# Performance work log

Hardware: AMD Instinct MI355X
Metric: run time of the kernel (lower is better)

## Reference

```python
import jax, jax.numpy as jnp
import numpy as np

VOCAB = 32000
HID = 1024


def _gru_cell(Wih, Whh, bih, bhh, h, x):
    # PyTorch GRU gate order: r, z, n
    gx = Wih @ x + bih          # [3H]
    gh = Whh @ h + bhh          # [3H]
    H = h.shape[0]
    r = jax.nn.sigmoid(gx[:H] + gh[:H])
    z = jax.nn.sigmoid(gx[H:2 * H] + gh[H:2 * H])
    n = jnp.tanh(gx[2 * H:] + r * gh[2 * H:])
    return (1.0 - z) * n + z * h


def setup_inputs() -> dict:
    key = jax.random.key(0)
    ks = jax.random.split(key, 13)
    S = 512
    T = 512
    s = 1.0 / np.sqrt(HID)
    u = lambda k, shape: jax.random.uniform(k, shape, jnp.float32, -s, s)
    return {
        "inputs": jax.random.randint(ks[0], (S,), 0, VOCAB, jnp.int32),
        "targets": jax.random.randint(ks[1], (T,), 0, VOCAB, jnp.int32),
        "emb": jax.random.normal(ks[2], (VOCAB, HID), jnp.float32),
        "enc_Wih": u(ks[3], (3 * HID, HID)),
        "enc_Whh": u(ks[4], (3 * HID, HID)),
        "enc_bih": u(ks[5], (3 * HID,)),
        "enc_bhh": u(ks[6], (3 * HID,)),
        "dec_Wih": u(ks[7], (3 * HID, HID)),
        "dec_Whh": u(ks[8], (3 * HID, HID)),
        "dec_bih": u(ks[9], (3 * HID,)),
        "dec_bhh": u(ks[10], (3 * HID,)),
        "proj_W": u(ks[11], (VOCAB, HID)),
        "proj_b": u(ks[12], (VOCAB,)),
    }


def reference(inputs, targets, emb, enc_Wih, enc_Whh, enc_bih, enc_bhh,
              dec_Wih, dec_Whh, dec_bih, dec_bhh, proj_W, proj_b):
    # Encoder: scan GRU over embedded source tokens (batch=1, state [H])
    src_emb = emb[inputs]  # [S,H]
    h0 = jnp.zeros((HID,), src_emb.dtype)

    def enc_step(h, x):
        return _gru_cell(enc_Wih, enc_Whh, enc_bih, enc_bhh, h, x), None

    enc_state, _ = jax.lax.scan(enc_step, h0, src_emb)

    # Decoder: teacher forcing; input token at step i is 0 (start) then targets[i-1]
    dec_tokens = jnp.concatenate([jnp.zeros((1,), targets.dtype), targets[:-1]])
    dec_emb = emb[dec_tokens]  # [T,H]

    def dec_step(h, x):
        h_new = _gru_cell(dec_Wih, dec_Whh, dec_bih, dec_bhh, h, x)
        return h_new, h_new

    _, dec_hs = jax.lax.scan(dec_step, enc_state, dec_emb)  # [T,H]

    # Projection to vocab logits (single GEMM over all timesteps)
    logits = dec_hs @ proj_W.T + proj_b  # [T,V]
    return logits
```

## Files before the change

kernel.cpp:

```cpp
#include <hip/hip_runtime.h>
#include <cstdint>
#include <cstddef>

#define H 1024
#define SEQ 512
#define THREEH 3072
#define VOCABN 32000
#define NBLK 64
#define NWORK 192
#define HPB 16

#define HBIAS 2.0f
#define HVALID 0.5f

template <int CTRL>
__device__ __forceinline__ float dpp_add(float v) {
    return v + __int_as_float(__builtin_amdgcn_update_dpp(
        0, __float_as_int(v), CTRL, 0xF, 0xF, true));
}
__device__ __forceinline__ float row16_sum(float v) {
    v = dpp_add<0xB1>(v);
    v = dpp_add<0x4E>(v);
    v = dpp_add<0x124>(v);
    v = dpp_add<0x128>(v);
    return v;
}

__device__ void rnn_path(int blk, int tid, float* smem,
    const float* __restrict__ eWhh, const float* __restrict__ ebhh,
    const float* __restrict__ dWhh, const float* __restrict__ dbhh,
    const float* __restrict__ gxe, const float* __restrict__ gxd,
    float* __restrict__ enc_t, float* __restrict__ dec_t,
    const float* __restrict__ fe, const float* __restrict__ fd)
{
    const int wave = tid >> 6;
    const int lane = tid & 63;
    const int g = lane >> 4;
    const int p = lane & 15;
    const int i0 = blk * HPB;
    const int myidx = i0 + 4 * wave + g;

    float* hs0 = smem;
    float* hs1 = smem + H;

    float4 wreg[3][16];
    float br, bz, bn;
    float hown = 0.f;

    auto load_w = [&](const float* __restrict__ W, const float* __restrict__ b) {
        float ws[3];
#pragma unroll
        for (int gate = 0; gate < 3; ++gate) {
            const float* base = W + (size_t)(gate * H + myidx) * H + 64 * p;
            float s = 0.f;
#pragma unroll
            for (int k = 0; k < 16; ++k) {
                float4 w = *(const float4*)(base + 4 * ((k + p) & 15));
                wreg[gate][k] = w;
                s += w.x + w.y + w.z + w.w;
            }
            ws[gate] = s;
        }
        br = b[myidx]         - HBIAS * row16_sum(ws[0]);
        bz = b[H + myidx]     - HBIAS * row16_sum(ws[1]);
        bn = b[2 * H + myidx] - HBIAS * row16_sum(ws[2]);
    };

    load_w(eWhh, ebhh);

    for (int step = 0; step < 2 * SEQ; ++step) {
        const bool dec = step >= SEQ;
        const int t = dec ? step - SEQ : step;
        if (dec && t == 0) load_w(dWhh, dbhh);

        if ((t & 63) == 0) {
            const float* fl = (dec ? fd : fe) + (t >> 6) * 64
                              + (lane < 48 ? lane : 47);
            for (;;) {
                float f = __hip_atomic_load(fl,
                    __ATOMIC_RELAXED, __HIP_MEMORY_SCOPE_AGENT);
                if (__all(f > HVALID)) break;
                __builtin_amdgcn_s_sleep(4);
            }
            __builtin_amdgcn_fence(__ATOMIC_ACQUIRE, "agent");
        }

        const float* gx = dec ? gxd : gxe;
        float* tb_out = (dec ? dec_t : enc_t) + (size_t)t * H;
        float* hb = (step & 1) ? hs1 : hs0;

        const float* gxp = gx + (size_t)t * THREEH + myidx;
        float gxr = gxp[0];
        float gxz = gxp[H];
        float gxn = gxp[2 * H];

        if (step == 0) {
            *(float4*)&hb[wave * 256 + lane * 4] =
                float4{HBIAS, HBIAS, HBIAS, HBIAS};
        } else {
            const float* tb_prev =
                (step <= SEQ) ? enc_t + (size_t)(step - 1) * H
                              : dec_t + (size_t)(step - SEQ - 1) * H;
            const unsigned long long* src =
                (const unsigned long long*)tb_prev + wave * 128 + lane * 2;
            union { unsigned long long u; float f[2]; } cv[2];
            for (;;) {
                cv[0].u = __hip_atomic_load(src,
                    __ATOMIC_RELAXED, __HIP_MEMORY_SCOPE_AGENT);
                cv[1].u = __hip_atomic_load(src + 1,
                    __ATOMIC_RELAXED, __HIP_MEMORY_SCOPE_AGENT);
                if ((cv[0].f[0] > HVALID) & (cv[0].f[1] > HVALID) &
                    (cv[1].f[0] > HVALID) & (cv[1].f[1] > HVALID)) break;
            }
            *(float4*)&hb[wave * 256 + lane * 4] =
                float4{cv[0].f[0], cv[0].f[1], cv[1].f[0], cv[1].f[1]};
        }
        __syncthreads();

        float a0 = 0.f, a1 = 0.f, a2 = 0.f;
#pragma unroll
        for (int k = 0; k < 16; ++k) {
            float4 h = *(const float4*)&hb[64 * p + 4 * ((k + p) & 15)];
            float4 w0 = wreg[0][k], w1 = wreg[1][k], w2 = wreg[2][k];
            a0 += w0.x * h.x + w0.y * h.y + w0.z * h.z + w0.w * h.w;
            a1 += w1.x * h.x + w1.y * h.y + w1.z * h.z + w1.w * h.w;
            a2 += w2.x * h.x + w2.y * h.y + w2.z * h.z + w2.w * h.w;
        }
        float sr = row16_sum(a0);
        float sz = row16_sum(a1);
        float sn = row16_sum(a2);

        float rg = 1.f / (1.f + expf(-(gxr + sr + br)));
        float zg = 1.f / (1.f + expf(-(gxz + sz + bz)));
        float ng = tanhf(gxn + rg * (sn + bn));
        float hnew = (1.f - zg) * ng + zg * hown;
        hown = hnew;

        if (p == 0)
            __hip_atomic_store(tb_out + myidx, hnew + HBIAS,
                               __ATOMIC_RELAXED, __HIP_MEMORY_SCOPE_AGENT);
    }
}

template <int MODE>
__device__ void gemm_tile(const float* __restrict__ Abase,
                          const int* __restrict__ toks,
                          int m0, int n0,
                          const float* __restrict__ W,
                          const float* __restrict__ bias,
                          float* __restrict__ C, int N,
                          float* __restrict__ sA, float* __restrict__ sB)
{
    const int tid = threadIdx.x;
    const int r = tid >> 2;
    const int c = tid & 3;
    const int tx = tid & 15;
    const int ty = tid >> 4;
    const int m = m0 + r;

    const float* Arow;
    if (MODE == 0)      Arow = Abase + (size_t)toks[m] * H;
    else if (MODE == 1) Arow = Abase + (size_t)(m == 0 ? 0 : toks[m - 1]) * H;
    else                Arow = Abase + (size_t)m * H;
    const float* Brow = W + (size_t)(n0 + r) * H;
    const float abias = (MODE == 2) ? HBIAS : 0.f;

    float acc[4][4] = {};
    for (int k0 = 0; k0 < H; k0 += 16) {
        float4 av = *(const float4*)(Arow + k0 + c * 4);
        float4 bv = *(const float4*)(Brow + k0 + c * 4);
        __syncthreads();
        sA[(c * 4 + 0) * 68 + r] = av.x - abias;
        sA[(c * 4 + 1) * 68 + r] = av.y - abias;
        sA[(c * 4 + 2) * 68 + r] = av.z - abias;
        sA[(c * 4 + 3) * 68 + r] = av.w - abias;
        sB[(c * 4 + 0) * 68 + r] = bv.x;
        sB[(c * 4 + 1) * 68 + r] = bv.y;
        sB[(c * 4 + 2) * 68 + r] = bv.z;
        sB[(c * 4 + 3) * 68 + r] = bv.w;
        __syncthreads();
#pragma unroll
        for (int kk = 0; kk < 16; ++kk) {
            float4 a = *(const float4*)&sA[kk * 68 + ty * 4];
            float4 b = *(const float4*)&sB[kk * 68 + tx * 4];
            float avv[4] = {a.x, a.y, a.z, a.w};
            float bvv[4] = {b.x, b.y, b.z, b.w};
#pragma unroll
            for (int i = 0; i < 4; ++i)
#pragma unroll
                for (int jj = 0; jj < 4; ++jj)
                    acc[i][jj] += avv[i] * bvv[jj];
        }
    }
    float4 bq = *(const float4*)(bias + n0 + tx * 4);
    float bb[4] = {bq.x, bq.y, bq.z, bq.w};
#pragma unroll
    for (int i = 0; i < 4; ++i) {
        float4 o;
        o.x = acc[i][0] + bb[0];
        o.y = acc[i][1] + bb[1];
        o.z = acc[i][2] + bb[2];
        o.w = acc[i][3] + bb[3];
        *(float4*)&C[(size_t)(m0 + ty * 4 + i) * N + n0 + tx * 4] = o;
    }
}

__device__ void worker_path(int wid, int tid, float* smem,
    const float* __restrict__ emb,
    const int* __restrict__ inputs, const int* __restrict__ targets,
    const float* __restrict__ eWih, const float* __restrict__ ebih,
    const float* __restrict__ dWih, const float* __restrict__ dbih,
    float* __restrict__ gxe, float* __restrict__ gxd,
    float* __restrict__ fe, float* __restrict__ fd,
    const float* __restrict__ dec_t,
    const float* __restrict__ pW, const float* __restrict__ pb,
    float* __restrict__ out)
{
    float* sA = smem;
    float* sB = smem + 16 * 68;

    for (int q = wid; q < 8 * 48; q += NWORK) {
        int mb = q / 48, nb = q % 48;
        gemm_tile<0>(emb, inputs, mb * 64, nb * 64, eWih, ebih,
                     gxe, THREEH, sA, sB);
        __threadfence();
        __syncthreads();
        if (tid == 0)
            __hip_atomic_store(fe + mb * 64 + nb, 1.0f,
                               __ATOMIC_RELAXED, __HIP_MEMORY_SCOPE_AGENT);
    }
    for (int q = wid; q < 8 * 48; q += NWORK) {
        int mb = q / 48, nb = q % 48;
        gemm_tile<1>(emb, targets, mb * 64, nb * 64, dWih, dbih,
                     gxd, THREEH, sA, sB);
        __threadfence();
        __syncthreads();
        if (tid == 0)
            __hip_atomic_store(fd + mb * 64 + nb, 1.0f,
                               __ATOMIC_RELAXED, __HIP_MEMORY_SCOPE_AGENT);
    }

    {
        float acc = 0.f;
        const size_t nlines = (size_t)VOCABN * H / 32;
        for (size_t i = (size_t)wid * 256 + tid; i < nlines;
             i += (size_t)NWORK * 256)
            acc += pW[i * 32];
        asm volatile("" :: "v"(acc));
    }

    int cur = -1;
    for (int tt = wid; tt < 8 * 500; tt += NWORK) {
        int mb = tt / 500, nb = tt % 500;
        if (mb != cur) {
            if (tid < 64) {
                const unsigned long long* src =
                    (const unsigned long long*)(dec_t + (size_t)(mb * 64 + 63) * H);
                for (;;) {
                    bool ok = true;
#pragma unroll
                    for (int m = 0; m < 8; ++m) {
                        union { unsigned long long u; float f[2]; } c;
                        c.u = __hip_atomic_load(src + tid + 64 * m,
                            __ATOMIC_RELAXED, __HIP_MEMORY_SCOPE_AGENT);
                        ok &= (c.f[0] > HVALID) & (c.f[1] > HVALID);
                    }
                    if (ok) break;
                    __builtin_amdgcn_s_sleep(64);
                }
            }
            __syncthreads();
            __builtin_amdgcn_fence(__ATOMIC_ACQUIRE, "agent");
            cur = mb;
        }
        gemm_tile<2>(dec_t, nullptr, mb * 64, nb * 64, pW, pb,
                     out, VOCABN, sA, sB);
    }
}

__global__ __launch_bounds__(256, 1) void fused_rnn(
    const float* __restrict__ eWhh, const float* __restrict__ ebhh,
    const float* __restrict__ dWhh, const float* __restrict__ dbhh,
    float* __restrict__ gxe, float* __restrict__ gxd,
    float* __restrict__ enc_t, float* __restrict__ dec_t,
    float* __restrict__ fe, float* __restrict__ fd,
    const float* __restrict__ emb,
    const int* __restrict__ inputs, const int* __restrict__ targets,
    const float* __restrict__ eWih, const float* __restrict__ ebih,
    const float* __restrict__ dWih, const float* __restrict__ dbih,
    const float* __restrict__ pW, const float* __restrict__ pb,
    float* __restrict__ out)
{
    __shared__ float smem[2176];
    const int b = blockIdx.x;
    if (b < NBLK)
        rnn_path(b, threadIdx.x, smem, eWhh, ebhh, dWhh, dbhh,
                 gxe, gxd, enc_t, dec_t, fe, fd);
    else
        worker_path(b - NBLK, threadIdx.x, smem, emb, inputs, targets,
                    eWih, ebih, dWih, dbih, gxe, gxd, fe, fd,
                    dec_t, pW, pb, out);
}

extern "C" void kernel_launch(void* const* d_in, const int* in_sizes, int n_in,
                              void* d_out, int out_size, void* d_ws, size_t ws_size,
                              hipStream_t stream) {
    const int*   inputs  = (const int*)d_in[0];
    const int*   targets = (const int*)d_in[1];
    const float* emb     = (const float*)d_in[2];
    const float* eWih    = (const float*)d_in[3];
    const float* eWhh    = (const float*)d_in[4];
    const float* ebih    = (const float*)d_in[5];
    const float* ebhh    = (const float*)d_in[6];
    const float* dWih    = (const float*)d_in[7];
    const float* dWhh    = (const float*)d_in[8];
    const float* dbih    = (const float*)d_in[9];
    const float* dbhh    = (const float*)d_in[10];
    const float* pW      = (const float*)d_in[11];
    const float* pb      = (const float*)d_in[12];
    float* out = (float*)d_out;

    float* gxe   = (float*)d_ws;
    float* gxd   = gxe + (size_t)SEQ * THREEH;
    float* enc_t = gxd + (size_t)SEQ * THREEH;
    float* dec_t = enc_t + (size_t)SEQ * H;
    float* fe    = dec_t + (size_t)SEQ * H;
    float* fd    = fe + 8 * 64;

    fused_rnn<<<NBLK + NWORK, 256, 0, stream>>>(
        eWhh, ebhh, dWhh, dbhh, gxe, gxd, enc_t, dec_t, fe, fd,
        emb, inputs, targets, eWih, ebih, dWih, dbih, pW, pb, out);
}
```

Measured before the change: 3.727 ms.

## Prefetch next-step input gates and split polling/storing lanes in GRU recurrence

```diff
diff --git a/kernel.cpp b/kernel.cpp
--- a/kernel.cpp
+++ b/kernel.cpp
@@ -68,54 +68,83 @@
 
     load_w(eWhh, ebhh);
 
+    float gxr, gxz, gxn;
+    {
+        const float* fl = fe + (lane < 48 ? lane : 47);
+        for (;;) {
+            float f = __hip_atomic_load(fl,
+                __ATOMIC_RELAXED, __HIP_MEMORY_SCOPE_AGENT);
+            if (__all(f > HVALID)) break;
+            __builtin_amdgcn_s_sleep(4);
+        }
+        __builtin_amdgcn_fence(__ATOMIC_ACQUIRE, "agent");
+        gxr = gxe[myidx];
+        gxz = gxe[H + myidx];
+        gxn = gxe[2 * H + myidx];
+    }
+
     for (int step = 0; step < 2 * SEQ; ++step) {
         const bool dec = step >= SEQ;
         const int t = dec ? step - SEQ : step;
         if (dec && t == 0) load_w(dWhh, dbhh);
 
-        if ((t & 63) == 0) {
-            const float* fl = (dec ? fd : fe) + (t >> 6) * 64
-                              + (lane < 48 ? lane : 47);
-            for (;;) {
-                float f = __hip_atomic_load(fl,
-                    __ATOMIC_RELAXED, __HIP_MEMORY_SCOPE_AGENT);
-                if (__all(f > HVALID)) break;
-                __builtin_amdgcn_s_sleep(4);
-            }
-            __builtin_amdgcn_fence(__ATOMIC_ACQUIRE, "agent");
-        }
-
-        const float* gx = dec ? gxd : gxe;
         float* tb_out = (dec ? dec_t : enc_t) + (size_t)t * H;
         float* hb = (step & 1) ? hs1 : hs0;
 
-        const float* gxp = gx + (size_t)t * THREEH + myidx;
-        float gxr = gxp[0];
-        float gxz = gxp[H];
-        float gxn = gxp[2 * H];
-
         if (step == 0) {
-            *(float4*)&hb[wave * 256 + lane * 4] =
-                float4{HBIAS, HBIAS, HBIAS, HBIAS};
-        } else {
+            if (lane < 32) {
+                *(float4*)&hb[wave * 256 + lane * 8] =
+                    float4{HBIAS, HBIAS, HBIAS, HBIAS};
+                *(float4*)&hb[wave * 256 + lane * 8 + 4] =
+                    float4{HBIAS, HBIAS, HBIAS, HBIAS};
+            }
+        } else if (lane < 32) {
             const float* tb_prev =
                 (step <= SEQ) ? enc_t + (size_t)(step - 1) * H
                               : dec_t + (size_t)(step - SEQ - 1) * H;
             const unsigned long long* src =
-                (const unsigned long long*)tb_prev + wave * 128 + lane * 2;
-            union { unsigned long long u; float f[2]; } cv[2];
+                (const unsigned long long*)tb_prev + wave * 128 + lane * 4;
+            union { unsigned long long u; float f[2]; } cv[4];
             for (;;) {
-                cv[0].u = __hip_atomic_load(src,
-                    __ATOMIC_RELAXED, __HIP_MEMORY_SCOPE_AGENT);
-                cv[1].u = __hip_atomic_load(src + 1,
-                    __ATOMIC_RELAXED, __HIP_MEMORY_SCOPE_AGENT);
-                if ((cv[0].f[0] > HVALID) & (cv[0].f[1] > HVALID) &
-                    (cv[1].f[0] > HVALID) & (cv[1].f[1] > HVALID)) break;
-            }
-            *(float4*)&hb[wave * 256 + lane * 4] =
+#pragma unroll
+                for (int q = 0; q < 4; ++q)
+                    cv[q].u = __hip_atomic_load(src + q,
+                        __ATOMIC_RELAXED, __HIP_MEMORY_SCOPE_AGENT);
+                bool ok = true;
+#pragma unroll
+                for (int q = 0; q < 4; ++q)
+                    ok &= (cv[q].f[0] > HVALID) & (cv[q].f[1] > HVALID);
+                if (ok) break;
+                __builtin_amdgcn_s_sleep(1);
+            }
+            *(float4*)&hb[wave * 256 + lane * 8] =
                 float4{cv[0].f[0], cv[0].f[1], cv[1].f[0], cv[1].f[1]};
-        }
-        __syncthreads();
+            *(float4*)&hb[wave * 256 + lane * 8 + 4] =
+                float4{cv[2].f[0], cv[2].f[1], cv[3].f[0], cv[3].f[1]};
+        }
+        __syncthreads();
+
+        float ngxr = 0.f, ngxz = 0.f, ngxn = 0.f;
+        if (step + 1 < 2 * SEQ) {
+            const bool dec1 = (step + 1) >= SEQ;
+            const int t1 = dec1 ? step + 1 - SEQ : step + 1;
+            if ((t1 & 63) == 0) {
+                const float* fl = (dec1 ? fd : fe) + (t1 >> 6) * 64
+                                  + (lane < 48 ? lane : 47);
+                for (;;) {
+                    float f = __hip_atomic_load(fl,
+                        __ATOMIC_RELAXED, __HIP_MEMORY_SCOPE_AGENT);
+                    if (__all(f > HVALID)) break;
+                    __builtin_amdgcn_s_sleep(4);
+                }
+                __builtin_amdgcn_fence(__ATOMIC_ACQUIRE, "agent");
+            }
+            const float* gxp = (dec1 ? gxd : gxe)
+                               + (size_t)t1 * THREEH + myidx;
+            ngxr = gxp[0];
+            ngxz = gxp[H];
+            ngxn = gxp[2 * H];
+        }
 
         float a0 = 0.f, a1 = 0.f, a2 = 0.f;
 #pragma unroll
@@ -136,9 +165,13 @@
         float hnew = (1.f - zg) * ng + zg * hown;
         hown = hnew;
 
-        if (p == 0)
-            __hip_atomic_store(tb_out + myidx, hnew + HBIAS,
+        float sv = __shfl(hnew, 16 * (lane & 3));
+        if (lane >= 32 && lane < 36)
+            __hip_atomic_store(tb_out + i0 + 4 * wave + (lane - 32),
+                               sv + HBIAS,
                                __ATOMIC_RELAXED, __HIP_MEMORY_SCOPE_AGENT);
+
+        gxr = ngxr; gxz = ngxz; gxn = ngxn;
     }
 }
 
```

Result: slower. 3.999 ms (+7.3%).
